# Performance work log

Hardware: AMD Instinct MI355X
Metric: run time of the kernel (lower is better)

The kernel has to match this reference:

```python
import jax, jax.numpy as jnp
import numpy as np

EPS = 1e-5
KQ_DIM = 512

def layer_norm(x, g, b):
    mu = jnp.mean(x, axis=-1, keepdims=True)
    var = jnp.mean((x - mu) ** 2, axis=-1, keepdims=True)
    return (x - mu) * jax.lax.rsqrt(var + EPS) * g + b

def setup_inputs() -> dict:
    key = jax.random.key(0)
    ks = jax.random.split(key, 8)
    B, Sq, Skv = 8, 2048, 2048
    vk_i_dim, q_i_dim, kq_dim = 512, 512, KQ_DIM
    vals = jax.random.normal(ks[0], (B, Skv, vk_i_dim), jnp.float32)
    keys = jax.random.normal(ks[1], (B, Skv, vk_i_dim), jnp.float32)
    ques = jax.random.normal(ks[2], (B, Sq, q_i_dim), jnp.float32)
    # causal: mask out strictly-upper triangle (future keys)
    causal_mask = jnp.triu(jnp.ones((Sq, Skv), jnp.bool_), k=1)
    key_mask = jnp.zeros((B, Skv), jnp.bool_)
    s = 1.0 / np.sqrt(vk_i_dim)
    Wv = jax.random.normal(ks[3], (vk_i_dim, q_i_dim), jnp.float32) * s
    Wk = jax.random.normal(ks[4], (vk_i_dim, kq_dim), jnp.float32) * s
    Wq = jax.random.normal(ks[5], (q_i_dim, kq_dim), jnp.float32) * (1.0 / np.sqrt(q_i_dim))
    return {
        "vals": vals, "keys": keys, "ques": ques,
        "causal_mask": causal_mask, "key_mask": key_mask,
        "Wv": Wv, "Wk": Wk, "Wq": Wq,
        "ln_k_g": jnp.ones((kq_dim,), jnp.float32), "ln_k_b": jnp.zeros((kq_dim,), jnp.float32),
        "ln_q_g": jnp.ones((kq_dim,), jnp.float32), "ln_q_b": jnp.zeros((kq_dim,), jnp.float32),
        "ln_o_g": jnp.ones((q_i_dim,), jnp.float32), "ln_o_b": jnp.zeros((q_i_dim,), jnp.float32),
    }

def reference(vals, keys, ques, causal_mask, key_mask, Wv, Wk, Wq,
              ln_k_g, ln_k_b, ln_q_g, ln_q_b, ln_o_g, ln_o_b):
    v = vals @ Wv                                   # [B, Skv, q_i_dim]
    k = layer_norm(keys @ Wk, ln_k_g, ln_k_b)       # [B, Skv, kq_dim]
    q = layer_norm(ques @ Wq, ln_q_g, ln_q_b)       # [B, Sq, kq_dim]
    a = jnp.einsum('bqd,bkd->bqk', q, k) / jnp.sqrt(jnp.asarray(KQ_DIM, q.dtype))
    neg_inf = jnp.asarray(-jnp.inf, a.dtype)
    a = jnp.where(causal_mask[None, :, :], neg_inf, a)
    a = jnp.where(key_mask[:, None, :], neg_inf, a)
    p = jax.nn.softmax(a, axis=-1)
    o = jnp.einsum('bqk,bkd->bqd', p, v)            # dropout = identity (eval)
    return layer_norm(o + ques, ln_o_g, ln_o_b)
```

## Files before the change

### kernel.cpp

```cpp
#include <hip/hip_runtime.h>
#include <cstdint>

typedef short bf8 __attribute__((ext_vector_type(8)));
typedef float f4 __attribute__((ext_vector_type(4)));

#define SEQ 2048
#define DIM 512
#define NMAT (512*512)
#define SCQ 0.04419417382415922f

__device__ inline unsigned short f2bf(float f){
    unsigned int u = __builtin_bit_cast(unsigned int, f);
    u = (u + 0x7FFFu + ((u >> 16) & 1u)) >> 16;
    return (unsigned short)u;
}

__device__ __forceinline__ void glds16(const unsigned short* gsrc, const unsigned short* ldst){
    __builtin_amdgcn_global_load_lds(
        (const __attribute__((address_space(1))) unsigned int*)gsrc,
        (__attribute__((address_space(3))) unsigned int*)ldst, 16, 0, 0);
}

__global__ void prep_w(const float* __restrict__ Wv, const float* __restrict__ Wk,
                       const float* __restrict__ Wq, unsigned short* __restrict__ Wt)
{
    const int m = blockIdx.y;
    const float* W = (m == 0) ? Wv : ((m == 1) ? Wk : Wq);
    const int o = blockIdx.x * 256 + threadIdx.x;
    const int n = o >> 9;
    const int k = o & 511;
    Wt[m * NMAT + o] = f2bf(W[k * 512 + n]);
}

__global__ __launch_bounds__(512, 1) void gemm3(
    const float* __restrict__ vals, const float* __restrict__ keys, const float* __restrict__ ques,
    const unsigned short* __restrict__ Wt,
    const float* __restrict__ kg, const float* __restrict__ kbe,
    const float* __restrict__ qg, const float* __restrict__ qbe,
    unsigned short* __restrict__ vt, unsigned short* __restrict__ kbuf, unsigned short* __restrict__ qbuf)
{
    __shared__ unsigned short a_lds[64 * DIM];
    float* red1    = (float*)a_lds;
    float* red2    = red1 + 512;
    float* stat_mu = red2 + 512;
    float* stat_rs = stat_mu + 64;

    const int tid = threadIdx.x;
    const int wv  = tid >> 6;
    const int l   = tid & 63;
    const int g   = l >> 4;
    const int lr  = l & 15;
    const int gid = blockIdx.x;
    const int m   = gid >> 8;
    const int r0  = (gid & 255) * 64;
    const float* X = (m == 0) ? vals : ((m == 1) ? keys : ques);
    const unsigned short* W = Wt + m * NMAT;

    {
        const int row = tid >> 3;
        const int cb  = (tid & 7) * 4;
        const float* xr = X + (size_t)(r0 + row) * DIM;
        #pragma unroll
        for (int i = 0; i < 16; ++i){
            const int col = cb + i * 32;
            const float4 v = *reinterpret_cast<const float4*>(xr + col);
            ushort4 h;
            h.x = f2bf(v.x); h.y = f2bf(v.y); h.z = f2bf(v.z); h.w = f2bf(v.w);
            const int byte = ((row * DIM + col) * 2) ^ ((row & 7) << 4);
            *reinterpret_cast<ushort4*>(reinterpret_cast<char*>(a_lds) + byte) = h;
        }
    }
    __syncthreads();

    f4 acc[4][4];
    #pragma unroll
    for (int i = 0; i < 4; ++i)
        #pragma unroll
        for (int j = 0; j < 4; ++j)
            acc[i][j] = (f4){0.f, 0.f, 0.f, 0.f};

    const int nb = wv * 64;
    #pragma unroll 4
    for (int ks = 0; ks < 16; ++ks){
        const int kof = ks * 32 + g * 8;
        bf8 af[4], bfr[4];
        #pragma unroll
        for (int rt = 0; rt < 4; ++rt){
            const int row = 16 * rt + lr;
            const int byte = ((row * DIM + kof) * 2) ^ ((row & 7) << 4);
            af[rt] = *reinterpret_cast<const bf8*>(reinterpret_cast<const char*>(a_lds) + byte);
        }
        #pragma unroll
        for (int ct = 0; ct < 4; ++ct)
            bfr[ct] = *reinterpret_cast<const bf8*>(W + (size_t)(nb + 16 * ct + lr) * DIM + kof);
        #pragma unroll
        for (int rt = 0; rt < 4; ++rt)
            #pragma unroll
            for (int ct = 0; ct < 4; ++ct)
                acc[rt][ct] = __builtin_amdgcn_mfma_f32_16x16x32_bf16(af[rt], bfr[ct], acc[rt][ct], 0, 0, 0);
    }

    if (m == 0){
        __syncthreads();
        #pragma unroll
        for (int rt = 0; rt < 4; ++rt)
            #pragma unroll
            for (int r = 0; r < 4; ++r){
                const int row = 16 * rt + g * 4 + r;
                #pragma unroll
                for (int ct = 0; ct < 4; ++ct){
                    const int d = nb + 16 * ct + lr;
                    const int byte = (d * 128 + row * 2) ^ ((d & 7) << 4);
                    *reinterpret_cast<unsigned short*>(reinterpret_cast<char*>(a_lds) + byte) = f2bf(acc[rt][ct][r]);
                }
            }
        __syncthreads();
        const int bb = r0 >> 11;
        const int s0 = r0 & 2047;
        #pragma unroll
        for (int pq = 0; pq < 4; ++pq){
            const int d  = pq * 128 + (tid >> 2);
            const int sc = (tid & 3) * 16;
            const int base = d * 128 + sc * 2;
            const int sw = (d & 7) << 4;
            const bf8 x0 = *reinterpret_cast<const bf8*>(reinterpret_cast<const char*>(a_lds) + (base ^ sw));
            const bf8 x1 = *reinterpret_cast<const bf8*>(reinterpret_cast<const char*>(a_lds) + ((base + 16) ^ sw));
            unsigned short* dst = vt + (size_t)(bb * 512 + d) * SEQ + s0 + sc;
            *reinterpret_cast<bf8*>(dst)     = x0;
            *reinterpret_cast<bf8*>(dst + 8) = x1;
        }
        return;
    }

    const float* gamma = (m == 1) ? kg  : qg;
    const float* beta  = (m == 1) ? kbe : qbe;
    const float scale  = (m == 1) ? 1.0f : SCQ;
    unsigned short* outp = (m == 1) ? kbuf : qbuf;

    __syncthreads();
    #pragma unroll
    for (int rt = 0; rt < 4; ++rt){
        #pragma unroll
        for (int r = 0; r < 4; ++r){
            float s1 = 0.f, s2 = 0.f;
            #pragma unroll
            for (int ct = 0; ct < 4; ++ct){ const float v = acc[rt][ct][r]; s1 += v; s2 += v * v; }
            #pragma unroll
            for (int mm = 1; mm < 16; mm <<= 1){ s1 += __shfl_xor(s1, mm, 64); s2 += __shfl_xor(s2, mm, 64); }
            if (lr == 0){
                const int row = 16 * rt + g * 4 + r;
                red1[row * 8 + wv] = s1;
                red2[row * 8 + wv] = s2;
            }
        }
    }
    __syncthreads();
    if (tid < 64){
        float S1 = 0.f, S2 = 0.f;
        #pragma unroll
        for (int w = 0; w < 8; ++w){ S1 += red1[tid * 8 + w]; S2 += red2[tid * 8 + w]; }
        const float mu = S1 * (1.0f / 512.0f);
        const float var = S2 * (1.0f / 512.0f) - mu * mu;
        stat_mu[tid] = mu;
        stat_rs[tid] = rsqrtf(var + 1e-5f);
    }
    __syncthreads();
    #pragma unroll
    for (int rt = 0; rt < 4; ++rt){
        #pragma unroll
        for (int r = 0; r < 4; ++r){
            const int row = 16 * rt + g * 4 + r;
            const float mu = stat_mu[row];
            const float rs = stat_rs[row];
            #pragma unroll
            for (int ct = 0; ct < 4; ++ct){
                const int d = nb + 16 * ct + lr;
                const float v = ((acc[rt][ct][r] - mu) * rs * gamma[d] + beta[d]) * scale;
                outp[(size_t)(r0 + row) * DIM + d] = f2bf(v);
            }
        }
    }
}

__global__ __launch_bounds__(512, 2) void attn(
    const unsigned short* __restrict__ qb, const unsigned short* __restrict__ kb,
    const unsigned short* __restrict__ vt, const float* __restrict__ qin,
    const float* __restrict__ g_o, const float* __restrict__ b_o,
    float* __restrict__ outp)
{
    __shared__ unsigned short k_lds[2 * 32 * DIM];
    __shared__ float s_lds[64][36];
    __shared__ unsigned short p_lds[64 * 64];
    __shared__ float m_lds[64], l_lds[64], fac_lds[64];
    __shared__ float red1[64 * 8], red2[64 * 8];
    __shared__ float stat_mu[64], stat_rs[64];

    const int tid = threadIdx.x;
    const int wv  = tid >> 6;
    const int l   = tid & 63;
    const int g   = l >> 4;
    const int lr  = l & 15;
    const int b   = blockIdx.x & 7;
    const int p   = blockIdx.x >> 3;
    const int q0a = 32 * p;
    const int q0b = 32 * (63 - p);
    const int n   = 64 - p;

    const int ct  = wv & 1;
    const int rt_ = wv >> 1;

    bf8 qf[16];
    {
        const int row = 16 * rt_ + lr;
        const int qglob = (row < 32) ? (q0a + row) : (q0b + row - 32);
        const unsigned short* qr = qb + (size_t)(b * SEQ + qglob) * DIM + g * 8;
        #pragma unroll
        for (int ks = 0; ks < 16; ++ks)
            qf[ks] = *reinterpret_cast<const bf8*>(qr + ks * 32);
    }

    auto kglds = [&](int it){
        const int bo = (it & 1) * (32 * DIM);
        #pragma unroll
        for (int i = 0; i < 4; ++i){
            const int row = 4 * wv + i;
            glds16(kb + (size_t)(b * SEQ + it * 32 + row) * DIM + ((l * 8) ^ ((row & 7) * 8)),
                   k_lds + bo + row * DIM);
        }
    };

    kglds(0);
    if (tid < 64){ m_lds[tid] = -__builtin_inff(); l_lds[tid] = 0.0f; }

    f4 acc[4][4];
    #pragma unroll
    for (int rt = 0; rt < 4; ++rt)
        #pragma unroll
        for (int cv = 0; cv < 4; ++cv)
            acc[rt][cv] = (f4){0.f, 0.f, 0.f, 0.f};
    bf8 vst[4];

    asm volatile("s_waitcnt vmcnt(0)" ::: "memory");
    __builtin_amdgcn_s_barrier();
    __builtin_amdgcn_sched_barrier(0);

    auto do_pv = [&](int itp){
        const bool frozen = (itp > p);
        #pragma unroll
        for (int rt = 0; rt < 4; ++rt){
            if (rt < 2 && frozen) continue;
            float f[4];
            #pragma unroll
            for (int r = 0; r < 4; ++r) f[r] = fac_lds[16 * rt + 4 * g + r];
            #pragma unroll
            for (int cv = 0; cv < 4; ++cv)
                #pragma unroll
                for (int r = 0; r < 4; ++r)
                    acc[rt][cv][r] *= f[r];
            const int prow = 16 * rt + lr;
            const bf8 pa = *reinterpret_cast<const bf8*>(
                reinterpret_cast<const char*>(p_lds) + prow * 128 + ((g * 16) ^ ((prow & 7) << 4)));
            #pragma unroll
            for (int cv = 0; cv < 4; ++cv)
                acc[rt][cv] = __builtin_amdgcn_mfma_f32_16x16x32_bf16(pa, vst[cv], acc[rt][cv], 0, 0, 0);
        }
    };

    for (int it = 0; it < n; ++it){
        const int k0 = it * 32;
        if (it + 1 < n) kglds(it + 1);

        if (it > 0) do_pv(it - 1);

        #pragma unroll
        for (int cv = 0; cv < 4; ++cv)
            vst[cv] = *reinterpret_cast<const bf8*>(
                vt + (size_t)(b * DIM + 64 * wv + 16 * cv + lr) * SEQ + k0 + g * 8);

        if (rt_ >= 2 || it <= p){
            const char* kbuf = reinterpret_cast<const char*>(k_lds) + (it & 1) * 32768;
            const int krow  = 16 * ct + lr;
            const int rbase = krow * 1024;
            const int rx    = (krow & 7) << 4;
            f4 sa[4];
            sa[0] = (f4){0.f,0.f,0.f,0.f}; sa[1] = (f4){0.f,0.f,0.f,0.f};
            sa[2] = (f4){0.f,0.f,0.f,0.f}; sa[3] = (f4){0.f,0.f,0.f,0.f};
            #pragma unroll
            for (int ks = 0; ks < 16; ++ks){
                const bf8 bk = *reinterpret_cast<const bf8*>(
                    kbuf + rbase + ((ks * 64 + g * 16) ^ rx));
                sa[ks & 3] = __builtin_amdgcn_mfma_f32_16x16x32_bf16(qf[ks], bk, sa[ks & 3], 0, 0, 0);
            }
            const f4 s = (sa[0] + sa[1]) + (sa[2] + sa[3]);
            const int srow = 16 * rt_ + 4 * g;
            #pragma unroll
            for (int r = 0; r < 4; ++r)
                s_lds[srow + r][16 * ct + lr] = s[r];
        }
        asm volatile("s_waitcnt lgkmcnt(0)" ::: "memory");
        __builtin_amdgcn_s_barrier();
        __builtin_amdgcn_sched_barrier(0);

        {
            const int row = tid >> 3;
            const int cp  = tid & 7;
            if (row >= 32 || it <= p){
                const float4 x0 = *reinterpret_cast<const float4*>(&s_lds[row][4 * cp]);
                float av[4] = {x0.x, x0.y, x0.z, x0.w};
                const int qrow = (row < 32) ? (q0a + row) : (q0b + row - 32);
                #pragma unroll
                for (int jj = 0; jj < 4; ++jj)
                    if (k0 + 4 * cp + jj > qrow) av[jj] = -1e30f;
                float pm = fmaxf(fmaxf(av[0], av[1]), fmaxf(av[2], av[3]));
                #pragma unroll
                for (int mm = 1; mm < 8; mm <<= 1) pm = fmaxf(pm, __shfl_xor(pm, mm, 64));
                const float mo = m_lds[row];
                const float mn = fmaxf(mo, pm);
                const float e0 = __expf(av[0] - mn), e1 = __expf(av[1] - mn);
                const float e2 = __expf(av[2] - mn), e3 = __expf(av[3] - mn);
                float ts = e0 + e1 + e2 + e3;
                #pragma unroll
                for (int mm = 1; mm < 8; mm <<= 1) ts += __shfl_xor(ts, mm, 64);
                if (cp == 0){
                    const float fc = __expf(mo - mn);
                    m_lds[row] = mn; fac_lds[row] = fc;
                    l_lds[row] = l_lds[row] * fc + ts;
                }
                uint2 pk;
                pk.x = (unsigned int)f2bf(e0) | ((unsigned int)f2bf(e1) << 16);
                pk.y = (unsigned int)f2bf(e2) | ((unsigned int)f2bf(e3) << 16);
                *reinterpret_cast<uint2*>(reinterpret_cast<char*>(p_lds) +
                    row * 128 + ((cp * 8) ^ ((row & 7) << 4))) = pk;
            }
        }
        asm volatile("s_waitcnt vmcnt(4)" ::: "memory");
        asm volatile("s_waitcnt lgkmcnt(0)" ::: "memory");
        __builtin_amdgcn_s_barrier();
        __builtin_amdgcn_sched_barrier(0);
    }

    asm volatile("s_waitcnt vmcnt(0)" ::: "memory");
    do_pv(n - 1);

    float li[4][4];
    #pragma unroll
    for (int rt = 0; rt < 4; ++rt)
        #pragma unroll
        for (int r = 0; r < 4; ++r)
            li[rt][r] = 1.0f / l_lds[16 * rt + 4 * g + r];
    #pragma unroll
    for (int rt = 0; rt < 4; ++rt){
        #pragma unroll
        for (int cv = 0; cv < 4; ++cv){
            #pragma unroll
            for (int r = 0; r < 4; ++r){
                const int row = 16 * rt + 4 * g + r;
                const int qglob = (row < 32) ? (q0a + row) : (q0b + row - 32);
                const int d = 64 * wv + 16 * cv + lr;
                acc[rt][cv][r] = acc[rt][cv][r] * li[rt][r]
                               + qin[(size_t)(b * SEQ + qglob) * DIM + d];
            }
        }
    }
    #pragma unroll
    for (int rt = 0; rt < 4; ++rt){
        #pragma unroll
        for (int r = 0; r < 4; ++r){
            float s1 = 0.f, s2 = 0.f;
            #pragma unroll
            for (int cv = 0; cv < 4; ++cv){ const float v = acc[rt][cv][r]; s1 += v; s2 += v * v; }
            #pragma unroll
            for (int mm = 1; mm < 16; mm <<= 1){ s1 += __shfl_xor(s1, mm, 64); s2 += __shfl_xor(s2, mm, 64); }
            if (lr == 0){
                const int row = 16 * rt + 4 * g + r;
                red1[row * 8 + wv] = s1;
                red2[row * 8 + wv] = s2;
            }
        }
    }
    __syncthreads();
    if (tid < 64){
        float S1 = 0.f, S2 = 0.f;
        #pragma unroll
        for (int w = 0; w < 8; ++w){ S1 += red1[tid * 8 + w]; S2 += red2[tid * 8 + w]; }
        const float mu = S1 * (1.0f / 512.0f);
        const float var = S2 * (1.0f / 512.0f) - mu * mu;
        stat_mu[tid] = mu;
        stat_rs[tid] = rsqrtf(var + 1e-5f);
    }
    __syncthreads();
    #pragma unroll
    for (int rt = 0; rt < 4; ++rt){
        #pragma unroll
        for (int r = 0; r < 4; ++r){
            const int row = 16 * rt + 4 * g + r;
            const int qglob = (row < 32) ? (q0a + row) : (q0b + row - 32);
            const float mu = stat_mu[row];
            const float rs = stat_rs[row];
            #pragma unroll
            for (int cv = 0; cv < 4; ++cv){
                const int d = 64 * wv + 16 * cv + lr;
                outp[(size_t)(b * SEQ + qglob) * DIM + d] =
                    (acc[rt][cv][r] - mu) * rs * g_o[d] + b_o[d];
            }
        }
    }
}

extern "C" void kernel_launch(void* const* d_in, const int* in_sizes, int n_in,
                              void* d_out, int out_size, void* d_ws, size_t ws_size,
                              hipStream_t stream)
{
    (void)in_sizes; (void)n_in; (void)out_size; (void)ws_size;
    const float* vals = (const float*)d_in[0];
    const float* keys = (const float*)d_in[1];
    const float* ques = (const float*)d_in[2];
    const float* Wv   = (const float*)d_in[5];
    const float* Wk   = (const float*)d_in[6];
    const float* Wq   = (const float*)d_in[7];
    const float* ln_k_g = (const float*)d_in[8];
    const float* ln_k_b = (const float*)d_in[9];
    const float* ln_q_g = (const float*)d_in[10];
    const float* ln_q_b = (const float*)d_in[11];
    const float* ln_o_g = (const float*)d_in[12];
    const float* ln_o_b = (const float*)d_in[13];
    float* outp = (float*)d_out;

    char* ws = (char*)d_ws;
    unsigned short* qbuf = (unsigned short*)(ws);
    unsigned short* kbuf = (unsigned short*)(ws + (size_t)16 * 1024 * 1024);
    unsigned short* vt   = (unsigned short*)(ws + (size_t)32 * 1024 * 1024);
    unsigned short* Wt   = (unsigned short*)(ws + (size_t)48 * 1024 * 1024);

    prep_w<<<dim3(1024, 3), 256, 0, stream>>>(Wv, Wk, Wq, Wt);

    gemm3<<<768, 512, 0, stream>>>(vals, keys, ques, Wt,
                                   ln_k_g, ln_k_b, ln_q_g, ln_q_b,
                                   vt, kbuf, qbuf);

    attn<<<256, 512, 0, stream>>>(qbuf, kbuf, vt, ques, ln_o_g, ln_o_b, outp);
}
```

Before: 197.8 us.

## Halve query rows per attention block and split QK^T over head-dim halves

The attention kernel now handles 32 query rows per block (16 from the front and 16 mirrored from the back) instead of 64, doubling the grid to 512 blocks. The QK^T product is split across wave pairs along the 512-wide feature dimension, and the partial scores are summed in a swizzled LDS buffer. Launch bounds are raised to 4 blocks per CU and LDS is trimmed by aliasing the reduction buffers onto the score buffer. The aim is more parallelism and occupancy so the causal work is better balanced across CUs. In exchange, K and V tiles are reloaded by twice as many blocks, and the extra partial-sum pass adds LDS traffic.

Measured after the change: 350.1 us. +76.9%, slower.

```diff
diff --git a/kernel.cpp b/kernel.cpp
--- a/kernel.cpp
+++ b/kernel.cpp
@@ -182,18 +182,20 @@
     }
 }
 
-__global__ __launch_bounds__(512, 2) void attn(
+__global__ __launch_bounds__(512, 4) void attn(
     const unsigned short* __restrict__ qb, const unsigned short* __restrict__ kb,
     const unsigned short* __restrict__ vt, const float* __restrict__ qin,
     const float* __restrict__ g_o, const float* __restrict__ b_o,
     float* __restrict__ outp)
 {
     __shared__ unsigned short k_lds[2 * 32 * DIM];
-    __shared__ float s_lds[64][36];
-    __shared__ unsigned short p_lds[64 * 64];
-    __shared__ float m_lds[64], l_lds[64], fac_lds[64];
-    __shared__ float red1[64 * 8], red2[64 * 8];
-    __shared__ float stat_mu[64], stat_rs[64];
+    __shared__ float s2_lds[2 * 32 * 32];
+    __shared__ unsigned short p_lds[32 * 64];
+    __shared__ float m_lds[32], l_lds[32], fac_lds[32];
+    float* red1    = s2_lds;
+    float* red2    = red1 + 256;
+    float* stat_mu = red2 + 256;
+    float* stat_rs = stat_mu + 32;
 
     const int tid = threadIdx.x;
     const int wv  = tid >> 6;
@@ -201,21 +203,22 @@
     const int g   = l >> 4;
     const int lr  = l & 15;
     const int b   = blockIdx.x & 7;
-    const int p   = blockIdx.x >> 3;
-    const int q0a = 32 * p;
-    const int q0b = 32 * (63 - p);
-    const int n   = 64 - p;
+    const int t   = blockIdx.x >> 3;
+    const int q0a = 16 * t;
+    const int q0b = 16 * (127 - t);
+    const int n   = ((2047 - 16 * t) >> 5) + 1;
+    const int tL  = (16 * t + 15) >> 5;
 
     const int ct  = wv & 1;
-    const int rt_ = wv >> 1;
-
-    bf8 qf[16];
+    const int kh  = (wv >> 1) & 1;
+    const int rt_ = wv >> 2;
+
+    bf8 qf[8];
     {
-        const int row = 16 * rt_ + lr;
-        const int qglob = (row < 32) ? (q0a + row) : (q0b + row - 32);
-        const unsigned short* qr = qb + (size_t)(b * SEQ + qglob) * DIM + g * 8;
-        #pragma unroll
-        for (int ks = 0; ks < 16; ++ks)
+        const int qglob = rt_ ? (q0b + lr) : (q0a + lr);
+        const unsigned short* qr = qb + (size_t)(b * SEQ + qglob) * DIM + kh * 256 + g * 8;
+        #pragma unroll
+        for (int ks = 0; ks < 8; ++ks)
             qf[ks] = *reinterpret_cast<const bf8*>(qr + ks * 32);
     }
 
@@ -230,25 +233,25 @@
     };
 
     kglds(0);
-    if (tid < 64){ m_lds[tid] = -__builtin_inff(); l_lds[tid] = 0.0f; }
-
-    f4 acc[4][4];
-    #pragma unroll
-    for (int rt = 0; rt < 4; ++rt)
+    if (tid < 32){ m_lds[tid] = -__builtin_inff(); l_lds[tid] = 0.0f; }
+
+    f4 acc[2][4];
+    #pragma unroll
+    for (int rt = 0; rt < 2; ++rt)
         #pragma unroll
         for (int cv = 0; cv < 4; ++cv)
             acc[rt][cv] = (f4){0.f, 0.f, 0.f, 0.f};
     bf8 vst[4];
 
-    asm volatile("s_waitcnt vmcnt(0)" ::: "memory");
+    asm volatile("s_waitcnt vmcnt(0) lgkmcnt(0)" ::: "memory");
     __builtin_amdgcn_s_barrier();
     __builtin_amdgcn_sched_barrier(0);
 
     auto do_pv = [&](int itp){
-        const bool frozen = (itp > p);
-        #pragma unroll
-        for (int rt = 0; rt < 4; ++rt){
-            if (rt < 2 && frozen) continue;
+        const bool frozen = (itp > tL);
+        #pragma unroll
+        for (int rt = 0; rt < 2; ++rt){
+            if (rt == 0 && frozen) continue;
             float f[4];
             #pragma unroll
             for (int r = 0; r < 4; ++r) f[r] = fac_lds[16 * rt + 4 * g + r];
@@ -277,7 +280,7 @@
             vst[cv] = *reinterpret_cast<const bf8*>(
                 vt + (size_t)(b * DIM + 64 * wv + 16 * cv + lr) * SEQ + k0 + g * 8);
 
-        if (rt_ >= 2 || it <= p){
+        if (rt_ == 1 || it <= tL){
             const char* kbuf = reinterpret_cast<const char*>(k_lds) + (it & 1) * 32768;
             const int krow  = 16 * ct + lr;
             const int rbase = krow * 1024;
@@ -286,28 +289,32 @@
             sa[0] = (f4){0.f,0.f,0.f,0.f}; sa[1] = (f4){0.f,0.f,0.f,0.f};
             sa[2] = (f4){0.f,0.f,0.f,0.f}; sa[3] = (f4){0.f,0.f,0.f,0.f};
             #pragma unroll
-            for (int ks = 0; ks < 16; ++ks){
+            for (int ks = 0; ks < 8; ++ks){
                 const bf8 bk = *reinterpret_cast<const bf8*>(
-                    kbuf + rbase + ((ks * 64 + g * 16) ^ rx));
+                    kbuf + rbase + (((kh * 8 + ks) * 64 + g * 16) ^ rx));
                 sa[ks & 3] = __builtin_amdgcn_mfma_f32_16x16x32_bf16(qf[ks], bk, sa[ks & 3], 0, 0, 0);
             }
             const f4 s = (sa[0] + sa[1]) + (sa[2] + sa[3]);
             const int srow = 16 * rt_ + 4 * g;
             #pragma unroll
-            for (int r = 0; r < 4; ++r)
-                s_lds[srow + r][16 * ct + lr] = s[r];
+            for (int r = 0; r < 4; ++r){
+                const int q = srow + r;
+                s2_lds[kh * 1024 + q * 32 + ((16 * ct + lr) ^ ((q & 7) << 2))] = s[r];
+            }
         }
         asm volatile("s_waitcnt lgkmcnt(0)" ::: "memory");
         __builtin_amdgcn_s_barrier();
         __builtin_amdgcn_sched_barrier(0);
 
-        {
+        if (tid < 256){
             const int row = tid >> 3;
             const int cp  = tid & 7;
-            if (row >= 32 || it <= p){
-                const float4 x0 = *reinterpret_cast<const float4*>(&s_lds[row][4 * cp]);
-                float av[4] = {x0.x, x0.y, x0.z, x0.w};
-                const int qrow = (row < 32) ? (q0a + row) : (q0b + row - 32);
+            if (row >= 16 || it <= tL){
+                const int swz = (row & 7) << 2;
+                const f4 x0 = *reinterpret_cast<const f4*>(&s2_lds[row * 32 + ((4 * cp) ^ swz)]);
+                const f4 x1 = *reinterpret_cast<const f4*>(&s2_lds[1024 + row * 32 + ((4 * cp) ^ swz)]);
+                float av[4] = {x0[0] + x1[0], x0[1] + x1[1], x0[2] + x1[2], x0[3] + x1[3]};
+                const int qrow = (row < 16) ? (q0a + row) : (q0b + row - 16);
                 #pragma unroll
                 for (int jj = 0; jj < 4; ++jj)
                     if (k0 + 4 * cp + jj > qrow) av[jj] = -1e30f;
@@ -342,20 +349,20 @@
     asm volatile("s_waitcnt vmcnt(0)" ::: "memory");
     do_pv(n - 1);
 
-    float li[4][4];
-    #pragma unroll
-    for (int rt = 0; rt < 4; ++rt)
+    float li[2][4];
+    #pragma unroll
+    for (int rt = 0; rt < 2; ++rt)
         #pragma unroll
         for (int r = 0; r < 4; ++r)
             li[rt][r] = 1.0f / l_lds[16 * rt + 4 * g + r];
     #pragma unroll
-    for (int rt = 0; rt < 4; ++rt){
+    for (int rt = 0; rt < 2; ++rt){
         #pragma unroll
         for (int cv = 0; cv < 4; ++cv){
             #pragma unroll
             for (int r = 0; r < 4; ++r){
                 const int row = 16 * rt + 4 * g + r;
-                const int qglob = (row < 32) ? (q0a + row) : (q0b + row - 32);
+                const int qglob = (row < 16) ? (q0a + row) : (q0b + row - 16);
                 const int d = 64 * wv + 16 * cv + lr;
                 acc[rt][cv][r] = acc[rt][cv][r] * li[rt][r]
                                + qin[(size_t)(b * SEQ + qglob) * DIM + d];
@@ -363,7 +370,7 @@
         }
     }
     #pragma unroll
-    for (int rt = 0; rt < 4; ++rt){
+    for (int rt = 0; rt < 2; ++rt){
         #pragma unroll
         for (int r = 0; r < 4; ++r){
             float s1 = 0.f, s2 = 0.f;
@@ -379,7 +386,7 @@
         }
     }
     __syncthreads();
-    if (tid < 64){
+    if (tid < 32){
         float S1 = 0.f, S2 = 0.f;
         #pragma unroll
         for (int w = 0; w < 8; ++w){ S1 += red1[tid * 8 + w]; S2 += red2[tid * 8 + w]; }
@@ -390,11 +397,11 @@
     }
     __syncthreads();
     #pragma unroll
-    for (int rt = 0; rt < 4; ++rt){
+    for (int rt = 0; rt < 2; ++rt){
         #pragma unroll
         for (int r = 0; r < 4; ++r){
             const int row = 16 * rt + 4 * g + r;
-            const int qglob = (row < 32) ? (q0a + row) : (q0b + row - 32);
+            const int qglob = (row < 16) ? (q0a + row) : (q0b + row - 16);
             const float mu = stat_mu[row];
             const float rs = stat_rs[row];
             #pragma unroll
@@ -438,5 +445,5 @@
                                    ln_k_g, ln_k_b, ln_q_g, ln_q_b,
                                    vt, kbuf, qbuf);
 
-    attn<<<256, 512, 0, stream>>>(qbuf, kbuf, vt, ques, ln_o_g, ln_o_b, outp);
-}
+    attn<<<512, 512, 0, stream>>>(qbuf, kbuf, vt, ques, ln_o_g, ln_o_b, outp);
+}
```

## Widen attention KV step to 64 keys with four-deep K buffering

Applied to the files above, without the earlier changes.

The attention main loop now handles 64 keys per iteration instead of 32, using two 32-key K tiles from a four-slot LDS ring and two P·V MFMAs per output tile. This halves the number of barrier-separated iterations and softmax rescaling passes, amortizing synchronization and online-softmax overhead. To fit the larger K buffer, the LDS reduction and statistics arrays are aliased onto the enlarged score buffer. The cost is more LDS and registers per block, which may threaten the two-blocks-per-CU occupancy target, plus coarser causal granularity that does some extra masked work.

Result: no change. 194.0 us (-1.9%).

```diff
diff --git a/kernel.cpp b/kernel.cpp
--- a/kernel.cpp
+++ b/kernel.cpp
@@ -188,12 +188,14 @@
     const float* __restrict__ g_o, const float* __restrict__ b_o,
     float* __restrict__ outp)
 {
-    __shared__ unsigned short k_lds[2 * 32 * DIM];
-    __shared__ float s_lds[64][36];
+    __shared__ unsigned short k_lds[4 * 32 * DIM];
+    __shared__ float s_lds[64][68];
     __shared__ unsigned short p_lds[64 * 64];
     __shared__ float m_lds[64], l_lds[64], fac_lds[64];
-    __shared__ float red1[64 * 8], red2[64 * 8];
-    __shared__ float stat_mu[64], stat_rs[64];
+    float* red1    = &s_lds[0][0];
+    float* red2    = red1 + 512;
+    float* stat_mu = red2 + 512;
+    float* stat_rs = stat_mu + 64;
 
     const int tid = threadIdx.x;
     const int wv  = tid >> 6;
@@ -204,7 +206,8 @@
     const int p   = blockIdx.x >> 3;
     const int q0a = 32 * p;
     const int q0b = 32 * (63 - p);
-    const int n   = 64 - p;
+    const int n2  = (65 - p) >> 1;
+    const int jL  = p >> 1;
 
     const int ct  = wv & 1;
     const int rt_ = wv >> 1;
@@ -219,17 +222,18 @@
             qf[ks] = *reinterpret_cast<const bf8*>(qr + ks * 32);
     }
 
-    auto kglds = [&](int it){
-        const int bo = (it & 1) * (32 * DIM);
+    auto kglds = [&](int t){
+        const int bo = (t & 3) * (32 * DIM);
         #pragma unroll
         for (int i = 0; i < 4; ++i){
             const int row = 4 * wv + i;
-            glds16(kb + (size_t)(b * SEQ + it * 32 + row) * DIM + ((l * 8) ^ ((row & 7) * 8)),
+            glds16(kb + (size_t)(b * SEQ + t * 32 + row) * DIM + ((l * 8) ^ ((row & 7) * 8)),
                    k_lds + bo + row * DIM);
         }
     };
 
     kglds(0);
+    kglds(1);
     if (tid < 64){ m_lds[tid] = -__builtin_inff(); l_lds[tid] = 0.0f; }
 
     f4 acc[4][4];
@@ -238,14 +242,14 @@
         #pragma unroll
         for (int cv = 0; cv < 4; ++cv)
             acc[rt][cv] = (f4){0.f, 0.f, 0.f, 0.f};
-    bf8 vst[4];
+    bf8 vst[8];
 
     asm volatile("s_waitcnt vmcnt(0)" ::: "memory");
     __builtin_amdgcn_s_barrier();
     __builtin_amdgcn_sched_barrier(0);
 
-    auto do_pv = [&](int itp){
-        const bool frozen = (itp > p);
+    auto do_pv = [&](int jp){
+        const bool frozen = (jp > jL);
         #pragma unroll
         for (int rt = 0; rt < 4; ++rt){
             if (rt < 2 && frozen) continue;
@@ -258,44 +262,56 @@
                 for (int r = 0; r < 4; ++r)
                     acc[rt][cv][r] *= f[r];
             const int prow = 16 * rt + lr;
-            const bf8 pa = *reinterpret_cast<const bf8*>(
-                reinterpret_cast<const char*>(p_lds) + prow * 128 + ((g * 16) ^ ((prow & 7) << 4)));
-            #pragma unroll
-            for (int cv = 0; cv < 4; ++cv)
-                acc[rt][cv] = __builtin_amdgcn_mfma_f32_16x16x32_bf16(pa, vst[cv], acc[rt][cv], 0, 0, 0);
+            const int sw = (prow & 7) << 4;
+            const bf8 pa0 = *reinterpret_cast<const bf8*>(
+                reinterpret_cast<const char*>(p_lds) + prow * 128 + ((g * 16) ^ sw));
+            const bf8 pa1 = *reinterpret_cast<const bf8*>(
+                reinterpret_cast<const char*>(p_lds) + prow * 128 + ((64 + g * 16) ^ sw));
+            #pragma unroll
+            for (int cv = 0; cv < 4; ++cv){
+                acc[rt][cv] = __builtin_amdgcn_mfma_f32_16x16x32_bf16(pa0, vst[2 * cv],     acc[rt][cv], 0, 0, 0);
+                acc[rt][cv] = __builtin_amdgcn_mfma_f32_16x16x32_bf16(pa1, vst[2 * cv + 1], acc[rt][cv], 0, 0, 0);
+            }
         }
     };
 
-    for (int it = 0; it < n; ++it){
-        const int k0 = it * 32;
-        if (it + 1 < n) kglds(it + 1);
-
-        if (it > 0) do_pv(it - 1);
+    for (int j = 0; j < n2; ++j){
+        const int k0 = 64 * j;
+        const int tp = 2 * j + 2;
+        if (tp     < 2 * n2) kglds(tp);
+        if (tp + 1 < 2 * n2) kglds(tp + 1);
+
+        if (j > 0) do_pv(j - 1);
 
         #pragma unroll
         for (int cv = 0; cv < 4; ++cv)
-            vst[cv] = *reinterpret_cast<const bf8*>(
-                vt + (size_t)(b * DIM + 64 * wv + 16 * cv + lr) * SEQ + k0 + g * 8);
-
-        if (rt_ >= 2 || it <= p){
-            const char* kbuf = reinterpret_cast<const char*>(k_lds) + (it & 1) * 32768;
+            #pragma unroll
+            for (int ks = 0; ks < 2; ++ks)
+                vst[2 * cv + ks] = *reinterpret_cast<const bf8*>(
+                    vt + (size_t)(b * DIM + 64 * wv + 16 * cv + lr) * SEQ + k0 + 32 * ks + g * 8);
+
+        if (rt_ >= 2 || j <= jL){
             const int krow  = 16 * ct + lr;
             const int rbase = krow * 1024;
             const int rx    = (krow & 7) << 4;
-            f4 sa[4];
-            sa[0] = (f4){0.f,0.f,0.f,0.f}; sa[1] = (f4){0.f,0.f,0.f,0.f};
-            sa[2] = (f4){0.f,0.f,0.f,0.f}; sa[3] = (f4){0.f,0.f,0.f,0.f};
-            #pragma unroll
-            for (int ks = 0; ks < 16; ++ks){
-                const bf8 bk = *reinterpret_cast<const bf8*>(
-                    kbuf + rbase + ((ks * 64 + g * 16) ^ rx));
-                sa[ks & 3] = __builtin_amdgcn_mfma_f32_16x16x32_bf16(qf[ks], bk, sa[ks & 3], 0, 0, 0);
-            }
-            const f4 s = (sa[0] + sa[1]) + (sa[2] + sa[3]);
-            const int srow = 16 * rt_ + 4 * g;
-            #pragma unroll
-            for (int r = 0; r < 4; ++r)
-                s_lds[srow + r][16 * ct + lr] = s[r];
+            #pragma unroll
+            for (int h = 0; h < 2; ++h){
+                const char* kbuf = reinterpret_cast<const char*>(k_lds) + ((2 * j + h) & 3) * 32768;
+                f4 sa[4];
+                sa[0] = (f4){0.f,0.f,0.f,0.f}; sa[1] = (f4){0.f,0.f,0.f,0.f};
+                sa[2] = (f4){0.f,0.f,0.f,0.f}; sa[3] = (f4){0.f,0.f,0.f,0.f};
+                #pragma unroll
+                for (int ks = 0; ks < 16; ++ks){
+                    const bf8 bk = *reinterpret_cast<const bf8*>(
+                        kbuf + rbase + ((ks * 64 + g * 16) ^ rx));
+                    sa[ks & 3] = __builtin_amdgcn_mfma_f32_16x16x32_bf16(qf[ks], bk, sa[ks & 3], 0, 0, 0);
+                }
+                const f4 s = (sa[0] + sa[1]) + (sa[2] + sa[3]);
+                const int srow = 16 * rt_ + 4 * g;
+                #pragma unroll
+                for (int r = 0; r < 4; ++r)
+                    s_lds[srow + r][32 * h + 16 * ct + lr] = s[r];
+            }
         }
         asm volatile("s_waitcnt lgkmcnt(0)" ::: "memory");
         __builtin_amdgcn_s_barrier();
@@ -304,21 +320,25 @@
         {
             const int row = tid >> 3;
             const int cp  = tid & 7;
-            if (row >= 32 || it <= p){
-                const float4 x0 = *reinterpret_cast<const float4*>(&s_lds[row][4 * cp]);
-                float av[4] = {x0.x, x0.y, x0.z, x0.w};
+            if (row >= 32 || j <= jL){
+                const float4 x0 = *reinterpret_cast<const float4*>(&s_lds[row][8 * cp]);
+                const float4 x1 = *reinterpret_cast<const float4*>(&s_lds[row][8 * cp + 4]);
+                float av[8] = {x0.x, x0.y, x0.z, x0.w, x1.x, x1.y, x1.z, x1.w};
                 const int qrow = (row < 32) ? (q0a + row) : (q0b + row - 32);
-                #pragma unroll
-                for (int jj = 0; jj < 4; ++jj)
-                    if (k0 + 4 * cp + jj > qrow) av[jj] = -1e30f;
-                float pm = fmaxf(fmaxf(av[0], av[1]), fmaxf(av[2], av[3]));
+                const int kc = k0 + 8 * cp;
+                #pragma unroll
+                for (int jj = 0; jj < 8; ++jj)
+                    if (kc + jj > qrow) av[jj] = -1e30f;
+                float pm = fmaxf(fmaxf(fmaxf(av[0], av[1]), fmaxf(av[2], av[3])),
+                                 fmaxf(fmaxf(av[4], av[5]), fmaxf(av[6], av[7])));
                 #pragma unroll
                 for (int mm = 1; mm < 8; mm <<= 1) pm = fmaxf(pm, __shfl_xor(pm, mm, 64));
                 const float mo = m_lds[row];
                 const float mn = fmaxf(mo, pm);
-                const float e0 = __expf(av[0] - mn), e1 = __expf(av[1] - mn);
-                const float e2 = __expf(av[2] - mn), e3 = __expf(av[3] - mn);
-                float ts = e0 + e1 + e2 + e3;
+                float e[8];
+                #pragma unroll
+                for (int jj = 0; jj < 8; ++jj) e[jj] = __expf(av[jj] - mn);
+                float ts = ((e[0] + e[1]) + (e[2] + e[3])) + ((e[4] + e[5]) + (e[6] + e[7]));
                 #pragma unroll
                 for (int mm = 1; mm < 8; mm <<= 1) ts += __shfl_xor(ts, mm, 64);
                 if (cp == 0){
@@ -326,21 +346,23 @@
                     m_lds[row] = mn; fac_lds[row] = fc;
                     l_lds[row] = l_lds[row] * fc + ts;
                 }
-                uint2 pk;
-                pk.x = (unsigned int)f2bf(e0) | ((unsigned int)f2bf(e1) << 16);
-                pk.y = (unsigned int)f2bf(e2) | ((unsigned int)f2bf(e3) << 16);
-                *reinterpret_cast<uint2*>(reinterpret_cast<char*>(p_lds) +
-                    row * 128 + ((cp * 8) ^ ((row & 7) << 4))) = pk;
-            }
-        }
-        asm volatile("s_waitcnt vmcnt(4)" ::: "memory");
+                uint4 pk;
+                pk.x = (unsigned int)f2bf(e[0]) | ((unsigned int)f2bf(e[1]) << 16);
+                pk.y = (unsigned int)f2bf(e[2]) | ((unsigned int)f2bf(e[3]) << 16);
+                pk.z = (unsigned int)f2bf(e[4]) | ((unsigned int)f2bf(e[5]) << 16);
+                pk.w = (unsigned int)f2bf(e[6]) | ((unsigned int)f2bf(e[7]) << 16);
+                *reinterpret_cast<uint4*>(reinterpret_cast<char*>(p_lds) +
+                    row * 128 + ((cp * 16) ^ ((row & 7) << 4))) = pk;
+            }
+        }
+        asm volatile("s_waitcnt vmcnt(8)" ::: "memory");
         asm volatile("s_waitcnt lgkmcnt(0)" ::: "memory");
         __builtin_amdgcn_s_barrier();
         __builtin_amdgcn_sched_barrier(0);
     }
 
     asm volatile("s_waitcnt vmcnt(0)" ::: "memory");
-    do_pv(n - 1);
+    do_pv(n2 - 1);
 
     float li[4][4];
     #pragma unroll
```
